# Performance work log

Measured on AMD Instinct MI355X. Metric: run time of the kernel, lower is better.

## Reference

```python
import jax, jax.numpy as jnp
import numpy as np

N = 100000
E = 1200000
D_IN, D_HID, D_OUT = 64, 64, 32


def setup_inputs() -> dict:
    key = jax.random.key(0)
    ks = jax.random.split(key, 8)
    x = jax.random.normal(ks[0], (N, D_IN), dtype=jnp.float32)
    edge_index = jax.random.randint(ks[1], (2, E), 0, N, dtype=jnp.int64)
    s_in = 1.0 / np.sqrt(D_IN)
    s_hid = 1.0 / np.sqrt(D_HID)
    return {
        "x": x,
        "edge_index": edge_index,
        "W1_l": jax.random.normal(ks[2], (D_IN, D_HID), dtype=jnp.float32) * s_in,
        "W1_r": jax.random.normal(ks[3], (D_IN, D_HID), dtype=jnp.float32) * s_in,
        "b1": jnp.zeros((D_HID,), dtype=jnp.float32),
        "W2_l": jax.random.normal(ks[4], (D_HID, D_OUT), dtype=jnp.float32) * s_hid,
        "W2_r": jax.random.normal(ks[5], (D_HID, D_OUT), dtype=jnp.float32) * s_hid,
        "b2": jnp.zeros((D_OUT,), dtype=jnp.float32),
    }


def _sage_conv(h, src, dst, W_l, W_r, b, n_nodes):
    # mean aggregation of source features onto destination nodes
    summed = jax.ops.segment_sum(h[src], dst, num_segments=n_nodes)  # [N, d]
    deg = jax.ops.segment_sum(jnp.ones((src.shape[0],), h.dtype), dst,
                              num_segments=n_nodes)  # [N]
    mean = summed / jnp.maximum(deg, 1.0)[:, None]
    # PyG SAGEConv: lin_l(aggr) + lin_r(x); bias lives on lin_l
    return mean @ W_l + b + h @ W_r


def reference(x, edge_index, W1_l, W1_r, b1, W2_l, W2_r, b2):
    src, dst = edge_index[0], edge_index[1]
    n = x.shape[0]
    h = jax.nn.relu(_sage_conv(x, src, dst, W1_l, W1_r, b1, n))
    return _sage_conv(h, src, dst, W2_l, W2_r, b2, n)
```

## Files before the change

### kernel.cpp

```cpp
#include <hip/hip_runtime.h>
#include <hip/hip_bf16.h>


#define D1 64
#define NQ 256
#define SUBN 391
#define QCAP 5632
#define LCAP 8448
#define BE 5120

static __device__ __forceinline__ float bf2f(ushort u) {
    unsigned int x = ((unsigned int)u) << 16;
    return __uint_as_float(x);
}
static __device__ __forceinline__ ushort f2bf(float f) {
    union { __hip_bfloat16 b; ushort u; } cv;
    cv.b = __float2bfloat16(f);
    return cv.u;
}
static __device__ __forceinline__ float lo2f(unsigned u) {
    return __uint_as_float(u << 16);
}
static __device__ __forceinline__ float hi2f(unsigned u) {
    return __uint_as_float(u & 0xffff0000u);
}
static __device__ __forceinline__ unsigned packbf(float x, float y) {
    return (unsigned)f2bf(x) | ((unsigned)f2bf(y) << 16);
}


__global__ __launch_bounds__(256)
void compact_edges256(const int* __restrict__ src, const int* __restrict__ dst,
                      int* __restrict__ tail, int2* __restrict__ queue, int E) {
    __shared__ int hist[NQ];
    __shared__ int base[NQ];
    int tid = threadIdx.x;
    int e0 = blockIdx.x * BE;
    int e1 = min(E, e0 + BE);

    hist[tid] = 0;
    __syncthreads();
    for (int e = e0 + tid; e < e1; e += 256)
        atomicAdd(&hist[dst[e] / SUBN], 1);
    __syncthreads();
    base[tid] = atomicAdd(&tail[tid], hist[tid]);
    hist[tid] = 0;
    __syncthreads();
    for (int e = e0 + tid; e < e1; e += 256) {
        int d = dst[e];
        int s = src[e];
        int p = d / SUBN;
        int pos = base[p] + atomicAdd(&hist[p], 1);
        if (pos < QCAP) queue[(size_t)p * QCAP + pos] = make_int2(s, d);
    }
}


__global__ __launch_bounds__(256)
void csr_build_local(const int2* __restrict__ queue, const int* __restrict__ tail,
                     int2* __restrict__ info, int* __restrict__ nbr, int N) {
    __shared__ int lcnt[512];
    __shared__ int psum[256];
    __shared__ int lnbr[LCAP];
    int tid = threadIdx.x;
    int p = blockIdx.x;
    int lo = p * SUBN;
    int nt = min(tail[p], QCAP);
    const int2* q = queue + (size_t)p * QCAP;
    int gbase = p * LCAP;

    lcnt[tid] = 0; lcnt[tid + 256] = 0;
    __syncthreads();
    for (int e = tid; e < nt; e += 256)
        atomicAdd(&lcnt[q[e].y - lo], 1);
    __syncthreads();

    int d0 = lcnt[2 * tid], d1 = lcnt[2 * tid + 1];
    int p0 = (d0 + 7) & ~7, p1 = (d1 + 7) & ~7;
    int s = p0 + p1;
    psum[tid] = s;
    __syncthreads();
    for (int off = 1; off < 256; off <<= 1) {
        int a = (tid >= off) ? psum[tid - off] : 0;
        __syncthreads();
        psum[tid] += a;
        __syncthreads();
    }
    int st0 = psum[tid] - s;
    int st1 = st0 + p0;
    int ptot = psum[255];

    {
        int li = 2 * tid, n = lo + li;
        if (li < SUBN && n < N) info[n] = make_int2(gbase + st0, d0);
        lcnt[li] = st0;
        li = 2 * tid + 1; n = lo + li;
        if (li < SUBN && n < N) info[n] = make_int2(gbase + st1, d1);
        lcnt[li] = st1;
    }
    __syncthreads();

    for (int e = tid; e < nt; e += 256) {
        int2 pr = q[e];
        int pos = atomicAdd(&lcnt[pr.y - lo], 1);
        lnbr[pos] = pr.x;
    }
    __syncthreads();

    for (int j = st0 + d0; j < st0 + p0; ++j) lnbr[j] = N;
    for (int j = st1 + d1; j < st1 + p1; ++j) lnbr[j] = N;
    __syncthreads();

    for (int i = tid; i < ptot; i += 256)
        nbr[gbase + i] = lnbr[i];
}


__global__ __launch_bounds__(256)
void cvt_bf16_init(const float* __restrict__ in, ushort* __restrict__ xh,
                   ushort* __restrict__ hh, int* __restrict__ tail,
                   int n4, int N) {
    int i = blockIdx.x * 256 + threadIdx.x;
    if (i < n4) {
        float4 v = *(const float4*)&in[(size_t)i * 4];
        ushort4 u;
        u.x = f2bf(v.x); u.y = f2bf(v.y); u.z = f2bf(v.z); u.w = f2bf(v.w);
        *(ushort4*)&xh[(size_t)i * 4] = u;
    }
    if (blockIdx.x == 0) tail[threadIdx.x] = 0;
    if (blockIdx.x == 1 && threadIdx.x < D1) {
        xh[(size_t)N * D1 + threadIdx.x] = 0;
        hh[(size_t)N * D1 + threadIdx.x] = 0;
    }
}


#define ACC8(u) do { \
    a0 += lo2f((u).x); a1 += hi2f((u).x); \
    a2 += lo2f((u).y); a3 += hi2f((u).y); \
    a4 += lo2f((u).z); a5 += hi2f((u).z); \
    a6 += lo2f((u).w); a7 += hi2f((u).w); } while (0)

__global__ __launch_bounds__(256)
void gather_mean8(const ushort* __restrict__ feat,
                  const int2* __restrict__ info,
                  const int* __restrict__ nbr,
                  ushort* __restrict__ mean, int N) {
    int wid  = (blockIdx.x * 256 + threadIdx.x) >> 6;
    int lane = threadIdx.x & 63;
    if (wid >= N) return;
    int2 ii = info[wid];
    int deg = ii.y;
    int m8 = (deg + 7) & ~7;
    const int* nb = nbr + ii.x;
    int r = lane >> 3;
    int c = lane & 7;
    const uint4* f4 = (const uint4*)feat;

    float a0 = 0, a1 = 0, a2 = 0, a3 = 0, a4 = 0, a5 = 0, a6 = 0, a7 = 0;
    int i = 0;
    for (; i + 16 <= m8; i += 16) {
        int e0 = nb[i + r];
        int e1 = nb[i + 8 + r];
        uint4 u0 = f4[(size_t)e0 * 8 + c];
        uint4 u1 = f4[(size_t)e1 * 8 + c];
        ACC8(u0);
        ACC8(u1);
    }
    if (i < m8) {
        int e0 = nb[i + r];
        uint4 u0 = f4[(size_t)e0 * 8 + c];
        ACC8(u0);
    }

    a0 += __shfl_xor(a0, 8, 64); a0 += __shfl_xor(a0, 16, 64); a0 += __shfl_xor(a0, 32, 64);
    a1 += __shfl_xor(a1, 8, 64); a1 += __shfl_xor(a1, 16, 64); a1 += __shfl_xor(a1, 32, 64);
    a2 += __shfl_xor(a2, 8, 64); a2 += __shfl_xor(a2, 16, 64); a2 += __shfl_xor(a2, 32, 64);
    a3 += __shfl_xor(a3, 8, 64); a3 += __shfl_xor(a3, 16, 64); a3 += __shfl_xor(a3, 32, 64);
    a4 += __shfl_xor(a4, 8, 64); a4 += __shfl_xor(a4, 16, 64); a4 += __shfl_xor(a4, 32, 64);
    a5 += __shfl_xor(a5, 8, 64); a5 += __shfl_xor(a5, 16, 64); a5 += __shfl_xor(a5, 32, 64);
    a6 += __shfl_xor(a6, 8, 64); a6 += __shfl_xor(a6, 16, 64); a6 += __shfl_xor(a6, 32, 64);
    a7 += __shfl_xor(a7, 8, 64); a7 += __shfl_xor(a7, 16, 64); a7 += __shfl_xor(a7, 32, 64);

    if (r == 0) {
        float inv = 1.0f / fmaxf((float)deg, 1.0f);
        uint4 o;
        o.x = packbf(a0 * inv, a1 * inv);
        o.y = packbf(a2 * inv, a3 * inv);
        o.z = packbf(a4 * inv, a5 * inv);
        o.w = packbf(a6 * inv, a7 * inv);
        ((uint4*)mean)[(size_t)wid * 8 + c] = o;
    }
}


#define TA_STRIDE 66

template <int DOUT, bool RELU, bool OUTBF>
__global__ __launch_bounds__(256)
void dense_sage(const ushort* __restrict__ Am,
                const ushort* __restrict__ Ax,
                const float* __restrict__ Wm,
                const float* __restrict__ Wx,
                const float* __restrict__ bias,
                void* __restrict__ outp, int N) {
    constexpr int JW = DOUT / 4;
    __shared__ char smraw[128 * TA_STRIDE * 2];
    ushort* ta = (ushort*)smraw;
    float*  to = (float*)smraw;

    int tid  = threadIdx.x;
    int w    = tid >> 6;
    int lane = tid & 63;
    int n0 = blockIdx.x * 64;

    #pragma unroll
    for (int i = 0; i < 8; ++i) {
        int flat = i * 256 + tid;
        int row  = flat >> 4;
        int c4   = (flat & 15) * 4;
        const ushort* A = (row < 64) ? Am : Ax;
        int node = row & 63;
        int grow = n0 + node;
        ushort4 u = make_ushort4(0, 0, 0, 0);
        if (grow < N) u = *(const ushort4*)&A[(size_t)grow * D1 + c4];
        int kb = ((row < 64) ? 0 : 64) + c4;
        ta[(kb + 0) * TA_STRIDE + node] = u.x;
        ta[(kb + 1) * TA_STRIDE + node] = u.y;
        ta[(kb + 2) * TA_STRIDE + node] = u.z;
        ta[(kb + 3) * TA_STRIDE + node] = u.w;
    }
    __syncthreads();

    int jb = __builtin_amdgcn_readfirstlane(w * JW);
    float c[JW];
    #pragma unroll
    for (int j = 0; j < JW; ++j) c[j] = bias[jb + j];

    #pragma unroll 4
    for (int k = 0; k < 64; ++k) {
        float a = bf2f(ta[k * TA_STRIDE + lane]);
        #pragma unroll
        for (int j = 0; j < JW; ++j)
            c[j] = fmaf(a, Wm[k * DOUT + jb + j], c[j]);
    }
    #pragma unroll 4
    for (int k = 0; k < 64; ++k) {
        float a = bf2f(ta[(64 + k) * TA_STRIDE + lane]);
        #pragma unroll
        for (int j = 0; j < JW; ++j)
            c[j] = fmaf(a, Wx[k * DOUT + jb + j], c[j]);
    }

    if (RELU) {
        #pragma unroll
        for (int j = 0; j < JW; ++j) c[j] = fmaxf(c[j], 0.0f);
    }

    __syncthreads();
    #pragma unroll
    for (int j = 0; j < JW; ++j) to[(jb + j) * 65 + lane] = c[j];
    __syncthreads();

    #pragma unroll
    for (int i = 0; i < DOUT / 16; ++i) {
        int flat = i * 256 + tid;
        int node = flat / (DOUT / 4);
        int q    = flat % (DOUT / 4);
        int grow = n0 + node;
        if (grow < N) {
            float vx = to[(q * 4 + 0) * 65 + node];
            float vy = to[(q * 4 + 1) * 65 + node];
            float vz = to[(q * 4 + 2) * 65 + node];
            float vw = to[(q * 4 + 3) * 65 + node];
            size_t o = (size_t)grow * DOUT + q * 4;
            if (OUTBF) {
                ushort4 u;
                u.x = f2bf(vx); u.y = f2bf(vy); u.z = f2bf(vz); u.w = f2bf(vw);
                *(ushort4*)&((ushort*)outp)[o] = u;
            } else {
                *(float4*)&((float*)outp)[o] = make_float4(vx, vy, vz, vw);
            }
        }
    }
}


extern "C" void kernel_launch(void* const* d_in, const int* in_sizes, int n_in,
                              void* d_out, int out_size, void* d_ws, size_t ws_size,
                              hipStream_t stream) {
    const float* x   = (const float*)d_in[0];
    const int*   ei  = (const int*)d_in[1];
    const float* W1l = (const float*)d_in[2];
    const float* W1r = (const float*)d_in[3];
    const float* b1  = (const float*)d_in[4];
    const float* W2l = (const float*)d_in[5];
    const float* W2r = (const float*)d_in[6];
    const float* b2  = (const float*)d_in[7];
    float* out = (float*)d_out;

    int N = in_sizes[0] / D1;
    int E = in_sizes[1] / 2;
    const int* src = ei;
    const int* dst = ei + E;

    char* ws = (char*)d_ws;
    auto alignup = [](size_t v) { return (v + 255) & ~(size_t)255; };
    size_t off = 0;
    int*    tail  = (int*)(ws + off);    off += alignup(NQ * 4);
    int2*   queue = (int2*)(ws + off);   off += alignup((size_t)NQ * QCAP * 8);
    int*    nbr   = (int*)(ws + off);    off += alignup((size_t)NQ * LCAP * 4);
    int2*   info  = (int2*)(ws + off);   off += alignup((size_t)N * 8);
    ushort* xh    = (ushort*)(ws + off); off += alignup((size_t)(N + 1) * D1 * 2);
    ushort* hh    = (ushort*)(ws + off); off += alignup((size_t)(N + 1) * D1 * 2);
    ushort* mean1 = (ushort*)d_out;
    ushort* mean2 = xh;

    int gb = (N + 3) / 4;
    int db = (N + 63) / 64;
    int cb = ((N * D1 / 4) + 255) / 256;
    int ab = (E + BE - 1) / BE;

    cvt_bf16_init<<<cb, 256, 0, stream>>>(x, xh, hh, tail, N * D1 / 4, N);
    compact_edges256<<<ab, 256, 0, stream>>>(src, dst, tail, queue, E);
    csr_build_local<<<NQ, 256, 0, stream>>>(queue, tail, info, nbr, N);

    gather_mean8<<<gb, 256, 0, stream>>>(xh, info, nbr, mean1, N);
    dense_sage<64, true, true ><<<db, 256, 0, stream>>>(mean1, xh, W1l, W1r, b1, hh, N);
    gather_mean8<<<gb, 256, 0, stream>>>(hh, info, nbr, mean2, N);
    dense_sage<32, false, false><<<db, 256, 0, stream>>>(mean2, hh, W2l, W2r, b2, out, N);
}
```

Baseline: 151.2 us.

## Project layer-2 features before aggregation to gather 32-wide rows instead of 64

Uses linearity of mean aggregation: layer 1's dense kernel now also computes h @ W2_l (32 columns, stored as bf16) so the second gather averages 32-wide rows instead of 64-wide ones. The layer-2 dense kernel then only applies W2_r and adds the pre-projected mean. Neighbor lists are padded to multiples of 16 to fit a new gather kernel with 16 rows per wave, which raises the per-bucket capacity. This halves the second gather's memory traffic but adds extra padding work and changes rounding order, since the projection is rounded to bf16 before averaging.

```diff
diff --git a/kernel.cpp b/kernel.cpp
--- a/kernel.cpp
+++ b/kernel.cpp
@@ -6,7 +6,7 @@
 #define NQ 256
 #define SUBN 391
 #define QCAP 5632
-#define LCAP 8448
+#define LCAP 11520
 #define BE 5120
 
 static __device__ __forceinline__ float bf2f(ushort u) {
@@ -76,7 +76,7 @@
     __syncthreads();
 
     int d0 = lcnt[2 * tid], d1 = lcnt[2 * tid + 1];
-    int p0 = (d0 + 7) & ~7, p1 = (d1 + 7) & ~7;
+    int p0 = (d0 + 15) & ~15, p1 = (d1 + 15) & ~15;
     int s = p0 + p1;
     psum[tid] = s;
     __syncthreads();
@@ -118,7 +118,7 @@
 
 __global__ __launch_bounds__(256)
 void cvt_bf16_init(const float* __restrict__ in, ushort* __restrict__ xh,
-                   ushort* __restrict__ hh, int* __restrict__ tail,
+                   ushort* __restrict__ y2, int* __restrict__ tail,
                    int n4, int N) {
     int i = blockIdx.x * 256 + threadIdx.x;
     if (i < n4) {
@@ -128,9 +128,9 @@
         *(ushort4*)&xh[(size_t)i * 4] = u;
     }
     if (blockIdx.x == 0) tail[threadIdx.x] = 0;
-    if (blockIdx.x == 1 && threadIdx.x < D1) {
-        xh[(size_t)N * D1 + threadIdx.x] = 0;
-        hh[(size_t)N * D1 + threadIdx.x] = 0;
+    if (blockIdx.x == 1) {
+        if (threadIdx.x < D1) xh[(size_t)N * D1 + threadIdx.x] = 0;
+        if (threadIdx.x < 32) y2[(size_t)N * 32 + threadIdx.x] = 0;
     }
 }
 
@@ -194,17 +194,71 @@
 }
 
 
+__global__ __launch_bounds__(256)
+void gather_mean16(const ushort* __restrict__ feat,
+                   const int2* __restrict__ info,
+                   const int* __restrict__ nbr,
+                   ushort* __restrict__ mean, int N) {
+    int wid  = (blockIdx.x * 256 + threadIdx.x) >> 6;
+    int lane = threadIdx.x & 63;
+    if (wid >= N) return;
+    int2 ii = info[wid];
+    int deg = ii.y;
+    int m16 = (deg + 15) & ~15;
+    const int* nb = nbr + ii.x;
+    int r = lane >> 2;
+    int c = lane & 3;
+    const uint4* f4 = (const uint4*)feat;
+
+    float a0 = 0, a1 = 0, a2 = 0, a3 = 0, a4 = 0, a5 = 0, a6 = 0, a7 = 0;
+    int i = 0;
+    for (; i + 32 <= m16; i += 32) {
+        int e0 = nb[i + r];
+        int e1 = nb[i + 16 + r];
+        uint4 u0 = f4[(size_t)e0 * 4 + c];
+        uint4 u1 = f4[(size_t)e1 * 4 + c];
+        ACC8(u0);
+        ACC8(u1);
+    }
+    if (i < m16) {
+        int e0 = nb[i + r];
+        uint4 u0 = f4[(size_t)e0 * 4 + c];
+        ACC8(u0);
+    }
+
+    a0 += __shfl_xor(a0, 4, 64); a0 += __shfl_xor(a0, 8, 64); a0 += __shfl_xor(a0, 16, 64); a0 += __shfl_xor(a0, 32, 64);
+    a1 += __shfl_xor(a1, 4, 64); a1 += __shfl_xor(a1, 8, 64); a1 += __shfl_xor(a1, 16, 64); a1 += __shfl_xor(a1, 32, 64);
+    a2 += __shfl_xor(a2, 4, 64); a2 += __shfl_xor(a2, 8, 64); a2 += __shfl_xor(a2, 16, 64); a2 += __shfl_xor(a2, 32, 64);
+    a3 += __shfl_xor(a3, 4, 64); a3 += __shfl_xor(a3, 8, 64); a3 += __shfl_xor(a3, 16, 64); a3 += __shfl_xor(a3, 32, 64);
+    a4 += __shfl_xor(a4, 4, 64); a4 += __shfl_xor(a4, 8, 64); a4 += __shfl_xor(a4, 16, 64); a4 += __shfl_xor(a4, 32, 64);
+    a5 += __shfl_xor(a5, 4, 64); a5 += __shfl_xor(a5, 8, 64); a5 += __shfl_xor(a5, 16, 64); a5 += __shfl_xor(a5, 32, 64);
+    a6 += __shfl_xor(a6, 4, 64); a6 += __shfl_xor(a6, 8, 64); a6 += __shfl_xor(a6, 16, 64); a6 += __shfl_xor(a6, 32, 64);
+    a7 += __shfl_xor(a7, 4, 64); a7 += __shfl_xor(a7, 8, 64); a7 += __shfl_xor(a7, 16, 64); a7 += __shfl_xor(a7, 32, 64);
+
+    if (r == 0) {
+        float inv = 1.0f / fmaxf((float)deg, 1.0f);
+        uint4 o;
+        o.x = packbf(a0 * inv, a1 * inv);
+        o.y = packbf(a2 * inv, a3 * inv);
+        o.z = packbf(a4 * inv, a5 * inv);
+        o.w = packbf(a6 * inv, a7 * inv);
+        ((uint4*)mean)[(size_t)wid * 4 + c] = o;
+    }
+}
+
+
 #define TA_STRIDE 66
 
-template <int DOUT, bool RELU, bool OUTBF>
-__global__ __launch_bounds__(256)
-void dense_sage(const ushort* __restrict__ Am,
-                const ushort* __restrict__ Ax,
-                const float* __restrict__ Wm,
-                const float* __restrict__ Wx,
-                const float* __restrict__ bias,
-                void* __restrict__ outp, int N) {
-    constexpr int JW = DOUT / 4;
+__global__ __launch_bounds__(256)
+void dense_sage1(const ushort* __restrict__ Am,
+                 const ushort* __restrict__ Ax,
+                 const float* __restrict__ Wm,
+                 const float* __restrict__ Wx,
+                 const float* __restrict__ bias,
+                 const float* __restrict__ W2l,
+                 ushort* __restrict__ hh,
+                 ushort* __restrict__ y2,
+                 int N) {
     __shared__ char smraw[128 * TA_STRIDE * 2];
     ushort* ta = (ushort*)smraw;
     float*  to = (float*)smraw;
@@ -232,55 +286,144 @@
     }
     __syncthreads();
 
-    int jb = __builtin_amdgcn_readfirstlane(w * JW);
-    float c[JW];
-    #pragma unroll
-    for (int j = 0; j < JW; ++j) c[j] = bias[jb + j];
+    int jb = __builtin_amdgcn_readfirstlane(w * 16);
+    float c[16];
+    #pragma unroll
+    for (int j = 0; j < 16; ++j) c[j] = bias[jb + j];
 
     #pragma unroll 4
     for (int k = 0; k < 64; ++k) {
         float a = bf2f(ta[k * TA_STRIDE + lane]);
         #pragma unroll
-        for (int j = 0; j < JW; ++j)
-            c[j] = fmaf(a, Wm[k * DOUT + jb + j], c[j]);
+        for (int j = 0; j < 16; ++j)
+            c[j] = fmaf(a, Wm[k * 64 + jb + j], c[j]);
     }
     #pragma unroll 4
     for (int k = 0; k < 64; ++k) {
         float a = bf2f(ta[(64 + k) * TA_STRIDE + lane]);
         #pragma unroll
-        for (int j = 0; j < JW; ++j)
-            c[j] = fmaf(a, Wx[k * DOUT + jb + j], c[j]);
-    }
-
-    if (RELU) {
-        #pragma unroll
-        for (int j = 0; j < JW; ++j) c[j] = fmaxf(c[j], 0.0f);
-    }
-
-    __syncthreads();
-    #pragma unroll
-    for (int j = 0; j < JW; ++j) to[(jb + j) * 65 + lane] = c[j];
-    __syncthreads();
-
-    #pragma unroll
-    for (int i = 0; i < DOUT / 16; ++i) {
+        for (int j = 0; j < 16; ++j)
+            c[j] = fmaf(a, Wx[k * 64 + jb + j], c[j]);
+    }
+    #pragma unroll
+    for (int j = 0; j < 16; ++j) c[j] = fmaxf(c[j], 0.0f);
+
+    __syncthreads();
+    #pragma unroll
+    for (int j = 0; j < 16; ++j) to[(jb + j) * 65 + lane] = c[j];
+    __syncthreads();
+
+    #pragma unroll
+    for (int i = 0; i < 4; ++i) {
         int flat = i * 256 + tid;
-        int node = flat / (DOUT / 4);
-        int q    = flat % (DOUT / 4);
+        int node = flat >> 4;
+        int q    = flat & 15;
         int grow = n0 + node;
         if (grow < N) {
-            float vx = to[(q * 4 + 0) * 65 + node];
-            float vy = to[(q * 4 + 1) * 65 + node];
-            float vz = to[(q * 4 + 2) * 65 + node];
-            float vw = to[(q * 4 + 3) * 65 + node];
-            size_t o = (size_t)grow * DOUT + q * 4;
-            if (OUTBF) {
-                ushort4 u;
-                u.x = f2bf(vx); u.y = f2bf(vy); u.z = f2bf(vz); u.w = f2bf(vw);
-                *(ushort4*)&((ushort*)outp)[o] = u;
-            } else {
-                *(float4*)&((float*)outp)[o] = make_float4(vx, vy, vz, vw);
-            }
+            ushort4 u;
+            u.x = f2bf(to[(q * 4 + 0) * 65 + node]);
+            u.y = f2bf(to[(q * 4 + 1) * 65 + node]);
+            u.z = f2bf(to[(q * 4 + 2) * 65 + node]);
+            u.w = f2bf(to[(q * 4 + 3) * 65 + node]);
+            *(ushort4*)&hh[(size_t)grow * D1 + q * 4] = u;
+        }
+    }
+
+    int jb2 = __builtin_amdgcn_readfirstlane(w * 8);
+    float c2[8];
+    #pragma unroll
+    for (int j = 0; j < 8; ++j) c2[j] = 0.0f;
+    #pragma unroll 4
+    for (int k = 0; k < 64; ++k) {
+        float a = to[k * 65 + lane];
+        #pragma unroll
+        for (int j = 0; j < 8; ++j)
+            c2[j] = fmaf(a, W2l[k * 32 + jb2 + j], c2[j]);
+    }
+    __syncthreads();
+    #pragma unroll
+    for (int j = 0; j < 8; ++j) to[(jb2 + j) * 65 + lane] = c2[j];
+    __syncthreads();
+
+    #pragma unroll
+    for (int i = 0; i < 2; ++i) {
+        int flat = i * 256 + tid;
+        int node = flat >> 3;
+        int q    = flat & 7;
+        int grow = n0 + node;
+        if (grow < N) {
+            ushort4 u;
+            u.x = f2bf(to[(q * 4 + 0) * 65 + node]);
+            u.y = f2bf(to[(q * 4 + 1) * 65 + node]);
+            u.z = f2bf(to[(q * 4 + 2) * 65 + node]);
+            u.w = f2bf(to[(q * 4 + 3) * 65 + node]);
+            *(ushort4*)&y2[(size_t)grow * 32 + q * 4] = u;
+        }
+    }
+}
+
+
+__global__ __launch_bounds__(256)
+void dense_sage2(const ushort* __restrict__ Ax,
+                 const ushort* __restrict__ mY2,
+                 const float* __restrict__ Wx,
+                 const float* __restrict__ bias,
+                 float* __restrict__ outp, int N) {
+    __shared__ char smraw[64 * TA_STRIDE * 2 + 32 * 65 * 4];
+    ushort* ta = (ushort*)smraw;
+    float*  to = (float*)(smraw + 64 * TA_STRIDE * 2);
+
+    int tid  = threadIdx.x;
+    int w    = tid >> 6;
+    int lane = tid & 63;
+    int n0 = blockIdx.x * 64;
+
+    #pragma unroll
+    for (int i = 0; i < 4; ++i) {
+        int flat = i * 256 + tid;
+        int row  = flat >> 4;
+        int c4   = (flat & 15) * 4;
+        int grow = n0 + row;
+        ushort4 u = make_ushort4(0, 0, 0, 0);
+        if (grow < N) u = *(const ushort4*)&Ax[(size_t)grow * D1 + c4];
+        ta[(c4 + 0) * TA_STRIDE + row] = u.x;
+        ta[(c4 + 1) * TA_STRIDE + row] = u.y;
+        ta[(c4 + 2) * TA_STRIDE + row] = u.z;
+        ta[(c4 + 3) * TA_STRIDE + row] = u.w;
+    }
+    __syncthreads();
+
+    int jb = __builtin_amdgcn_readfirstlane(w * 8);
+    float c[8];
+    #pragma unroll
+    for (int j = 0; j < 8; ++j) c[j] = bias[jb + j];
+
+    #pragma unroll 4
+    for (int k = 0; k < 64; ++k) {
+        float a = bf2f(ta[k * TA_STRIDE + lane]);
+        #pragma unroll
+        for (int j = 0; j < 8; ++j)
+            c[j] = fmaf(a, Wx[k * 32 + jb + j], c[j]);
+    }
+
+    #pragma unroll
+    for (int j = 0; j < 8; ++j) to[(jb + j) * 65 + lane] = c[j];
+    __syncthreads();
+
+    #pragma unroll
+    for (int i = 0; i < 2; ++i) {
+        int flat = i * 256 + tid;
+        int node = flat >> 3;
+        int q    = flat & 7;
+        int grow = n0 + node;
+        if (grow < N) {
+            ushort4 m = *(const ushort4*)&mY2[(size_t)grow * 32 + q * 4];
+            float4 v;
+            v.x = to[(q * 4 + 0) * 65 + node] + bf2f(m.x);
+            v.y = to[(q * 4 + 1) * 65 + node] + bf2f(m.y);
+            v.z = to[(q * 4 + 2) * 65 + node] + bf2f(m.z);
+            v.w = to[(q * 4 + 3) * 65 + node] + bf2f(m.w);
+            *(float4*)&outp[(size_t)grow * 32 + q * 4] = v;
         }
     }
 }
@@ -313,20 +456,21 @@
     int2*   info  = (int2*)(ws + off);   off += alignup((size_t)N * 8);
     ushort* xh    = (ushort*)(ws + off); off += alignup((size_t)(N + 1) * D1 * 2);
     ushort* hh    = (ushort*)(ws + off); off += alignup((size_t)(N + 1) * D1 * 2);
-    ushort* mean1 = (ushort*)d_out;
-    ushort* mean2 = xh;
+    ushort* y2    = (ushort*)(ws + off); off += alignup((size_t)(N + 1) * 32 * 2);
+    ushort* mean1  = (ushort*)d_out;
+    ushort* meanY2 = xh;
 
     int gb = (N + 3) / 4;
     int db = (N + 63) / 64;
     int cb = ((N * D1 / 4) + 255) / 256;
     int ab = (E + BE - 1) / BE;
 
-    cvt_bf16_init<<<cb, 256, 0, stream>>>(x, xh, hh, tail, N * D1 / 4, N);
+    cvt_bf16_init<<<cb, 256, 0, stream>>>(x, xh, y2, tail, N * D1 / 4, N);
     compact_edges256<<<ab, 256, 0, stream>>>(src, dst, tail, queue, E);
     csr_build_local<<<NQ, 256, 0, stream>>>(queue, tail, info, nbr, N);
 
     gather_mean8<<<gb, 256, 0, stream>>>(xh, info, nbr, mean1, N);
-    dense_sage<64, true, true ><<<db, 256, 0, stream>>>(mean1, xh, W1l, W1r, b1, hh, N);
-    gather_mean8<<<gb, 256, 0, stream>>>(hh, info, nbr, mean2, N);
-    dense_sage<32, false, false><<<db, 256, 0, stream>>>(mean2, hh, W2l, W2r, b2, out, N);
-}
+    dense_sage1<<<db, 256, 0, stream>>>(mean1, xh, W1l, W1r, b1, W2l, hh, y2, N);
+    gather_mean16<<<gb, 256, 0, stream>>>(y2, info, nbr, meanY2, N);
+    dense_sage2<<<db, 256, 0, stream>>>(hh, meanY2, W2r, b2, out, N);
+}
```

Result: slower. 156.7 us (+3.6%).
